# Performance work log

Hardware: AMD Instinct MI355X
Metric: run time of the kernel (lower is better)

Reference implementation:

```python
import jax, jax.numpy as jnp
import numpy as np

N, E, G = 100000, 400000, 4096
H, C = 4, 32            # heads, hidden_dim per head
D_OUT = H * C           # 128
NODE_D, EDGE_D = 38, 13
DEC_H, OUT_D = 64, 1
NEG_SLOPE = 0.2
LN_EPS = 1e-5


def setup_inputs() -> dict:
    key = jax.random.key(0)
    ks = jax.random.split(key, 40)
    r = lambda k, s: jax.random.normal(k, s, jnp.float32) * 0.1
    inp = {
        "x": jax.random.normal(ks[0], (N, NODE_D), jnp.float32),
        "edge_index": jax.random.randint(ks[1], (2, E), 0, N),
        "edge_attr": jax.random.uniform(ks[2], (E, EDGE_D), jnp.float32),
        "batch": jnp.sort(jax.random.randint(ks[3], (N,), 0, G)),
        # --- block 1 (in=38) ---
        "Wl1": r(ks[4], (NODE_D, D_OUT)), "bl1": jnp.zeros((D_OUT,), jnp.float32),
        "Wr1": r(ks[5], (NODE_D, D_OUT)), "br1": jnp.zeros((D_OUT,), jnp.float32),
        "We1": r(ks[6], (EDGE_D, D_OUT)),
        "att1": r(ks[7], (H, C)), "ab1": jnp.zeros((D_OUT,), jnp.float32),
        "ln_g1": jnp.ones((D_OUT,), jnp.float32), "ln_b1": jnp.zeros((D_OUT,), jnp.float32),
        "Wres": r(ks[8], (NODE_D, D_OUT)), "bres": jnp.zeros((D_OUT,), jnp.float32),
        # --- block 2 (in=128, residual = identity) ---
        "Wl2": r(ks[9], (D_OUT, D_OUT)), "bl2": jnp.zeros((D_OUT,), jnp.float32),
        "Wr2": r(ks[10], (D_OUT, D_OUT)), "br2": jnp.zeros((D_OUT,), jnp.float32),
        "We2": r(ks[11], (EDGE_D, D_OUT)),
        "att2": r(ks[12], (H, C)), "ab2": jnp.zeros((D_OUT,), jnp.float32),
        "ln_g2": jnp.ones((D_OUT,), jnp.float32), "ln_b2": jnp.zeros((D_OUT,), jnp.float32),
        # --- readout MLP ---
        "Wd1": r(ks[13], (D_OUT, DEC_H)), "bd1": jnp.zeros((DEC_H,), jnp.float32),
        "Wd2": r(ks[14], (DEC_H, OUT_D)), "bd2": jnp.zeros((OUT_D,), jnp.float32),
    }
    return inp


def _segment_softmax(logits, seg, n):
    m = jax.ops.segment_max(logits, seg, num_segments=n)
    ex = jnp.exp(logits - m[seg])
    s = jax.ops.segment_sum(ex, seg, num_segments=n)
    return ex / s[seg]


def _gatv2(x, src, dst, e_feat, Wl, bl, Wr, br, We, att, ab):
    n = x.shape[0]
    xl = (x @ Wl + bl).reshape(n, H, C)   # source transform
    xr = (x @ Wr + br).reshape(n, H, C)   # target transform
    ee = (e_feat @ We).reshape(-1, H, C)  # edge transform
    z = jax.nn.leaky_relu(xl[src] + xr[dst] + ee, NEG_SLOPE)  # [E,H,C]
    logits = jnp.einsum('ehc,hc->eh', z, att)                 # [E,H]
    alpha = _segment_softmax(logits, dst, n)                  # softmax over target nbhd
    out = jax.ops.segment_sum(xl[src] * alpha[..., None], dst, num_segments=n)
    return out.reshape(n, D_OUT) + ab


def _layernorm(h, g, b):
    mu = jnp.mean(h, -1, keepdims=True)
    d = h - mu
    v = jnp.mean(d * d, -1, keepdims=True)
    return d * jax.lax.rsqrt(v + LN_EPS) * g + b


def reference(x, edge_index, edge_attr, batch,
              Wl1, bl1, Wr1, br1, We1, att1, ab1, ln_g1, ln_b1, Wres, bres,
              Wl2, bl2, Wr2, br2, We2, att2, ab2, ln_g2, ln_b2,
              Wd1, bd1, Wd2, bd2):
    src, dst = edge_index[0], edge_index[1]
    n = x.shape[0]
    # add_self_loops(fill_value='mean'): self-loop edge attr = mean of incoming edge attrs
    deg = jax.ops.segment_sum(jnp.ones((src.shape[0],), x.dtype), dst, num_segments=n)
    loop_attr = jax.ops.segment_sum(edge_attr, dst, num_segments=n) / jnp.clip(deg, 1.0)[:, None]
    nodes = jnp.arange(n)
    src_a = jnp.concatenate([src, nodes])
    dst_a = jnp.concatenate([dst, nodes])
    ea = jnp.concatenate([edge_attr, loop_attr], axis=0)

    # block 1
    h = _gatv2(x, src_a, dst_a, ea, Wl1, bl1, Wr1, br1, We1, att1, ab1)
    h = jax.nn.elu(h)
    h = _layernorm(h + (x @ Wres + bres), ln_g1, ln_b1)
    # block 2 (identity residual)
    h2 = _gatv2(h, src_a, dst_a, ea, Wl2, bl2, Wr2, br2, We2, att2, ab2)
    h2 = jax.nn.elu(h2)
    h2 = _layernorm(h2 + h, ln_g2, ln_b2)

    # global mean pool over graphs
    cnt = jax.ops.segment_sum(jnp.ones((n,), x.dtype), batch, num_segments=G)
    g = jax.ops.segment_sum(h2, batch, num_segments=G) / jnp.clip(cnt, 1.0)[:, None]

    return jax.nn.relu(g @ Wd1 + bd1) @ Wd2 + bd2
```

## Files before the change

kernel.cpp:

```cpp
#include <hip/hip_runtime.h>

typedef unsigned short u16;
typedef unsigned int   u32;
typedef __attribute__((ext_vector_type(8))) short short8;
typedef __attribute__((ext_vector_type(4))) float float4v;
typedef __attribute__((ext_vector_type(2))) float float2v;
typedef __attribute__((ext_vector_type(4), aligned(4))) float float4u;

#define NODE_D   38
#define EDGE_D   13
#define D_OUT    128
#define NEG_SLOPE 0.2f
#define LN_EPS   1e-5f

__device__ __forceinline__ float bf2f(u16 v) { return __uint_as_float(((u32)v) << 16); }
__device__ __forceinline__ u16 f2bf(float f) {
    u32 u = __float_as_uint(f);
    u += 0x7fffu + ((u >> 16) & 1u);
    return (u16)(u >> 16);
}

template <int CTRL>
__device__ __forceinline__ float dpp_radd(float x) {
    int t = __builtin_amdgcn_update_dpp(0, __float_as_int(x), CTRL, 0xf, 0xf, true);
    return x + __int_as_float(t);
}
__device__ __forceinline__ float reduce16(float p) {
    p = dpp_radd<0xB1>(p);
    p = dpp_radd<0x4E>(p);
    p = dpp_radd<0x124>(p);
    p = dpp_radd<0x128>(p);
    return p;
}
__device__ __forceinline__ float reduce64(float v) {
    v = reduce16(v);
    v += __shfl_xor(v, 16, 64);
    v += __shfl_xor(v, 32, 64);
    return v;
}

__global__ void k_pre(const int* __restrict__ dst, int E, int* __restrict__ deg,
                      const int* __restrict__ batch, int N, int G, int* __restrict__ goff,
                      const float* __restrict__ x, u16* __restrict__ xb) {
    int i = blockIdx.x * blockDim.x + threadIdx.x;
    if (i < E) atomicAdd(deg + dst[i], 1);
    if (i < N) {
        int b = batch[i];
        int prev = (i == 0) ? -1 : batch[i - 1];
        for (int g = prev + 1; g <= b; g++) goff[g] = i;
        if (i == N - 1)
            for (int g = b + 1; g <= G; g++) goff[g] = N;
    }
    if (i < N * 32) {
        int n = i >> 5, kk = (i & 31) * 2;
        float f0 = 0.f, f1 = 0.f;
        if (kk < NODE_D) {
            float2v v = *(const float2v*)(x + (size_t)n * NODE_D + kk);
            f0 = v[0]; f1 = v[1];
        }
        ((u32*)xb)[(size_t)n * 32 + (i & 31)] = (u32)f2bf(f0) | ((u32)f2bf(f1) << 16);
    }
}

#define SCAN_CHUNK 1024
__global__ void k_scan1(const int* __restrict__ cnt, int N, int addone, int* __restrict__ bsum) {
    __shared__ int sh[256];
    int base = blockIdx.x * SCAN_CHUNK;
    int t = threadIdx.x;
    int s = 0;
#pragma unroll
    for (int i = 0; i < 4; i++) { int idx = base + t * 4 + i; if (idx < N) s += cnt[idx] + addone; }
    sh[t] = s; __syncthreads();
    for (int ofs = 128; ofs > 0; ofs >>= 1) {
        if (t < ofs) sh[t] += sh[t + ofs];
        __syncthreads();
    }
    if (t == 0) bsum[blockIdx.x] = sh[0];
}
__global__ void k_scan2(const int* __restrict__ bsum, int nb, int* __restrict__ boff) {
    __shared__ int sh[256];
    int t = threadIdx.x;
    if (nb <= 256) {
        int v = (t < nb) ? bsum[t] : 0;
        sh[t] = v; __syncthreads();
        for (int ofs = 1; ofs < 256; ofs <<= 1) {
            int x = (t >= ofs) ? sh[t - ofs] : 0;
            __syncthreads();
            sh[t] += x;
            __syncthreads();
        }
        if (t < nb) boff[t] = sh[t] - v;
        if (t == nb - 1) boff[nb] = sh[t];
    } else if (t == 0) {
        int run = 0;
        for (int i = 0; i < nb; i++) { boff[i] = run; run += bsum[i]; }
        boff[nb] = run;
    }
}
__global__ void k_scan3(const int* __restrict__ cnt, int N, int addone,
                        const int* __restrict__ boff, int nb, int* __restrict__ off) {
    __shared__ int wtot[4];
    int base = blockIdx.x * SCAN_CHUNK;
    int t = threadIdx.x;
    int lane = t & 63, w = t >> 6;
    int v[4]; int s = 0;
#pragma unroll
    for (int i = 0; i < 4; i++) { int idx = base + t * 4 + i; v[i] = (idx < N) ? cnt[idx] + addone : 0; s += v[i]; }
    int inc = s;
#pragma unroll
    for (int ofs = 1; ofs < 64; ofs <<= 1) {
        int x = __shfl_up(inc, ofs, 64);
        if (lane >= ofs) inc += x;
    }
    if (lane == 63) wtot[w] = inc;
    __syncthreads();
    int wofs = 0;
    for (int i = 0; i < w; i++) wofs += wtot[i];
    int run = boff[blockIdx.x] + wofs + (inc - s);
#pragma unroll
    for (int i = 0; i < 4; i++) {
        int idx = base + t * 4 + i;
        if (idx < N) off[idx] = run;
        run += v[i];
    }
    if (blockIdx.x == 0 && t == 0) off[N] = boff[nb];
}

__global__ void k_fill(const int* __restrict__ src, const int* __restrict__ dst,
                       const float* __restrict__ eattr, int E,
                       const int* __restrict__ csr_off, int* __restrict__ fill,
                       int* __restrict__ csr_src, u16* __restrict__ A) {
    int e = blockIdx.x * blockDim.x + threadIdx.x;
    if (e >= E) return;
    int d = dst[e];
    int pos = csr_off[d] + atomicAdd(fill + d, 1);
    csr_src[pos] = src[e];
    const float* ep = eattr + (size_t)e * EDGE_D;
    float4u v0 = *(const float4u*)(ep);
    float4u v1 = *(const float4u*)(ep + 4);
    float4u v2 = *(const float4u*)(ep + 8);
    float   v3 = ep[12];
    u16 row[16];
#pragma unroll
    for (int k = 0; k < 4; k++) { row[k] = f2bf(v0[k]); row[4 + k] = f2bf(v1[k]); row[8 + k] = f2bf(v2[k]); }
    row[12] = f2bf(v3);
#pragma unroll
    for (int k = EDGE_D; k < 16; k++) row[k] = 0;
    uint4* rp = (uint4*)(A + (size_t)pos * 16);
    rp[0] = (uint4){(u32)row[0] | ((u32)row[1] << 16), (u32)row[2] | ((u32)row[3] << 16),
                    (u32)row[4] | ((u32)row[5] << 16), (u32)row[6] | ((u32)row[7] << 16)};
    rp[1] = (uint4){(u32)row[8] | ((u32)row[9] << 16), (u32)row[10] | ((u32)row[11] << 16),
                    (u32)row[12] | ((u32)row[13] << 16), (u32)row[14] | ((u32)row[15] << 16)};
}

__global__ __launch_bounds__(256) void k_self(const int* __restrict__ csr_off, int N,
                                              int* __restrict__ csr_src, u16* __restrict__ A) {
    int wave = blockIdx.x * 4 + (threadIdx.x >> 6);
    if (wave >= N) return;
    int lane = threadIdx.x & 63;
    int r = lane >> 4, k = lane & 15;
    int b = csr_off[wave], e2 = csr_off[wave + 1] - 1;
    float s = 0.f;
    for (int j = b + r; j < e2; j += 4)
        s += bf2f(A[(size_t)j * 16 + k]);
    s += __shfl_xor(s, 16, 64);
    s += __shfl_xor(s, 32, 64);
    if (lane < 16) {
        u16 v = (k < EDGE_D) ? f2bf(s / fmaxf((float)(e2 - b), 1.f)) : (u16)0;
        A[(size_t)e2 * 16 + k] = v;
        if (k == 0) csr_src[e2] = wave;
    }
}

template <int KPAD, int CT, int KREAL, bool IN_BF16>
__global__ __launch_bounds__(256) void k_tf_mfma(
    const void* __restrict__ in_v,
    const float* __restrict__ W0, const float* __restrict__ b0,
    const float* __restrict__ W1, const float* __restrict__ b1,
    const float* __restrict__ W2, const float* __restrict__ b2,
    u16* __restrict__ o0, u16* __restrict__ o1, u16* __restrict__ o2,
    int N) {
    constexpr int RS = KPAD + 8;
    __shared__ u16 Bsw[CT * 16 * RS];
    __shared__ float bsh[CT * 16];
    const float* Ws[3] = {W0, W1, W2};
    const float* bs[3] = {b0, b1, b2};
    u16* outs[3] = {o0, o1, o2};
    int t = threadIdx.x;
    for (int i = t; i < CT * 16 * KPAD; i += 256) {
        int c = i / KPAD, k = i - c * KPAD;
        float v = (k < KREAL) ? Ws[c >> 7][(size_t)k * 128 + (c & 127)] : 0.f;
        Bsw[c * RS + k] = f2bf(v);
    }
    for (int i = t; i < CT * 16; i += 256) bsh[i] = bs[i >> 7][i & 127];
    __syncthreads();

    int wid = t >> 6, lane = t & 63;
    int quad = lane >> 4, m = lane & 15;

    for (int g0 = blockIdx.x * 64; g0 < N; g0 += gridDim.x * 64) {
        int na = g0 + wid * 16 + m;
        if (na > N - 1) na = N - 1;
        short8 a[KPAD / 32];
        if (IN_BF16) {
            const u16* in = (const u16*)in_v;
#pragma unroll
            for (int kc = 0; kc < KPAD / 32; kc++)
                a[kc] = *(const short8*)(in + (size_t)na * KPAD + kc * 32 + quad * 8);
        } else {
            const float* in = (const float*)in_v;
#pragma unroll
            for (int kc = 0; kc < KPAD / 32; kc++)
#pragma unroll
                for (int j = 0; j < 8; j++) {
                    int k = kc * 32 + quad * 8 + j;
                    float v = (k < KREAL) ? in[(size_t)na * KREAL + k] : 0.f;
                    a[kc][j] = (short)f2bf(v);
                }
        }
        float4v acc[CT];
#pragma unroll
        for (int ct = 0; ct < CT; ct++) acc[ct] = (float4v){0.f, 0.f, 0.f, 0.f};
#pragma unroll
        for (int ct = 0; ct < CT; ct++) {
#pragma unroll
            for (int kc = 0; kc < KPAD / 32; kc++) {
                short8 b = *(const short8*)(&Bsw[(ct * 16 + m) * RS + kc * 32 + quad * 8]);
                acc[ct] = __builtin_amdgcn_mfma_f32_16x16x32_bf16(b, a[kc], acc[ct], 0, 0, 0);
            }
        }
        int node = g0 + wid * 16 + m;
        if (node < N) {
#pragma unroll
            for (int ct = 0; ct < CT; ct++) {
                int colb = ct * 16 + quad * 4;
                u16* op = outs[colb >> 7];
                int cc = colb & 127;
                float4v bq = *(const float4v*)&bsh[colb];
                ushort4 wv;
                wv.x = f2bf(acc[ct][0] + bq[0]);
                wv.y = f2bf(acc[ct][1] + bq[1]);
                wv.z = f2bf(acc[ct][2] + bq[2]);
                wv.w = f2bf(acc[ct][3] + bq[3]);
                *(ushort4*)(op + (size_t)node * 128 + cc) = wv;
            }
        }
    }
}

template <bool POOL>
__global__ __launch_bounds__(256) void k_gat(
    const int* __restrict__ csr_off, const int* __restrict__ csr_src,
    const u16* __restrict__ A_csr,
    const u16* __restrict__ xl, const u16* __restrict__ xr,
    const u16* __restrict__ res, const float* __restrict__ We,
    const float* __restrict__ att, const float* __restrict__ ab,
    const float* __restrict__ lng, const float* __restrict__ lnb,
    u16* __restrict__ hout, const int* __restrict__ batch, float* __restrict__ gsum,
    int N, int npw) {
    int t = threadIdx.x;
    int wid = t >> 6, lane = t & 63;
    int nb = gridDim.x, b = blockIdx.x;
    int q = nb >> 3, r = nb & 7;
    int xcd = b & 7, ib = b >> 3;
    int swz = (xcd < r ? xcd * (q + 1) : r * (q + 1) + (xcd - r) * q) + ib;
    int wave = swz * 4 + wid;
    int n0 = wave * npw;
    if (n0 >= N) return;
    int n1 = n0 + npw; if (n1 > N) n1 = N;

    float2v we2[EDGE_D];
#pragma unroll
    for (int k = 0; k < EDGE_D; k++)
        we2[k] = (float2v){We[k * D_OUT + 2 * lane], We[k * D_OUT + 2 * lane + 1]};
    float a0 = att[2 * lane], a1 = att[2 * lane + 1];
    float abv0 = ab[2 * lane], abv1 = ab[2 * lane + 1];
    float lg0 = lng[2 * lane], lg1 = lng[2 * lane + 1];
    float lb0 = lnb[2 * lane], lb1 = lnb[2 * lane + 1];

    const u32* xl32 = (const u32*)xl;
    const u32* xr32 = (const u32*)xr;
    int wbeg = csr_off[n0];
    int wend = csr_off[n1];
    int nedge = wend - wbeg;

    float ps0 = 0.f, ps1 = 0.f;
    int gcur = POOL ? batch[n0] : -1;

    auto finish = [&](int n, float ssum, float2v acc2) {
        float inv = 1.f / ssum;
        float o0 = acc2[0] * inv + abv0;
        float o1 = acc2[1] * inv + abv1;
        o0 = (o0 > 0.f) ? o0 : (__expf(o0) - 1.f);
        o1 = (o1 > 0.f) ? o1 : (__expf(o1) - 1.f);
        u32 rw = ((const u32*)res)[(size_t)n * 64 + lane];
        o0 += bf2f((u16)(rw & 0xffff));
        o1 += bf2f((u16)(rw >> 16));
        float sm = reduce64(o0 + o1);
        float mu = sm * (1.f / 128.f);
        float d0 = o0 - mu, d1 = o1 - mu;
        float vv = reduce64(d0 * d0 + d1 * d1);
        float rs = rsqrtf(vv * (1.f / 128.f) + LN_EPS);
        float h0 = d0 * rs * lg0 + lb0;
        float h1 = d1 * rs * lg1 + lb1;
        if (POOL) {
            int g = batch[n];
            if (g != gcur) {
                atomicAdd(gsum + (size_t)gcur * 128 + 2 * lane, ps0);
                atomicAdd(gsum + (size_t)gcur * 128 + 2 * lane + 1, ps1);
                ps0 = 0.f; ps1 = 0.f; gcur = g;
            }
            ps0 += h0; ps1 += h1;
        } else {
            ((u32*)hout)[(size_t)n * 64 + lane] = (u32)f2bf(h0) | ((u32)f2bf(h1) << 16);
        }
    };

    const float2v z0v = (float2v){0.f, 0.f};

    if (nedge <= 64) {
        int last = nedge - 1;
        int sv = csr_src[wbeg + ((lane < nedge) ? lane : last)];
        int f0 = __builtin_amdgcn_readlane(sv, 0);
        int f1 = __builtin_amdgcn_readlane(sv, (1 <= last) ? 1 : last);
        int f2 = __builtin_amdgcn_readlane(sv, (2 <= last) ? 2 : last);
        int f3 = __builtin_amdgcn_readlane(sv, (3 <= last) ? 3 : last);
        u32 xw0 = xl32[(size_t)f0 * 64 + lane];
        u32 xw1 = xl32[(size_t)f1 * 64 + lane];
        u32 xw2 = xl32[(size_t)f2 * 64 + lane];
        u32 xw3 = xl32[(size_t)f3 * 64 + lane];
        int wbu = __builtin_amdgcn_readfirstlane(wbeg);
        const uint4* ap = (const uint4*)(A_csr + (size_t)wbu * 16);
        uint4 aq0 = ap[0], aq1 = ap[1];

        int i = wbeg;
        for (int n = n0; n < n1; n++) {
            int end = csr_off[n + 1];
            u32 xrw = xr32[(size_t)n * 64 + lane];
            float2v xr2 = (float2v){bf2f((u16)(xrw & 0xffff)), bf2f((u16)(xrw >> 16))};
            float ssum = 0.f;
            float2v acc2 = (float2v){0.f, 0.f};
            for (; i < end; i++) {
                int j4 = i + 4 - wbeg; if (j4 > last) j4 = last;
                int f4 = __builtin_amdgcn_readlane(sv, j4);
                u32 xwN = xl32[(size_t)f4 * 64 + lane];
                int j1n = i + 1 - wbeg; if (j1n > last) j1n = last;
                int ipu = __builtin_amdgcn_readfirstlane(wbeg + j1n);
                const uint4* apn = (const uint4*)(A_csr + (size_t)ipu * 16);
                uint4 an0 = apn[0], an1 = apn[1];

                u32 dw[8] = {aq0.x, aq0.y, aq0.z, aq0.w, aq1.x, aq1.y, aq1.z, aq1.w};
                float2v eeA = (float2v){0.f, 0.f}, eeB = (float2v){0.f, 0.f};
#pragma unroll
                for (int k = 0; k < EDGE_D; k++) {
                    u32 d = dw[k >> 1];
                    float av = __uint_as_float((k & 1) ? (d & 0xffff0000u) : (d << 16));
                    if ((k >> 1) & 1) eeB += we2[k] * av;
                    else             eeA += we2[k] * av;
                }
                float2v xs = (float2v){bf2f((u16)(xw0 & 0xffff)), bf2f((u16)(xw0 >> 16))};
                float2v z = (xs + xr2) + (eeA + eeB);
                float2v lz = __builtin_elementwise_max(z, z0v) + __builtin_elementwise_min(z, z0v) * NEG_SLOPE;
                float p = lz[0] * a0 + lz[1] * a1;
                p = reduce16(p);
                float wgt = __expf(p);
                ssum += wgt;
                acc2 += xs * wgt;
                xw0 = xw1; xw1 = xw2; xw2 = xw3; xw3 = xwN;
                aq0 = an0; aq1 = an1;
            }
            finish(n, ssum, acc2);
        }
    } else {
        int cl = wend - 1;
        int f = csr_src[wbeg];
        u32 xw = xl32[(size_t)f * 64 + lane];
        int wbu = __builtin_amdgcn_readfirstlane(wbeg);
        const uint4* ap = (const uint4*)(A_csr + (size_t)wbu * 16);
        uint4 aq0 = ap[0], aq1 = ap[1];
        int i = wbeg;
        for (int n = n0; n < n1; n++) {
            int end = csr_off[n + 1];
            u32 xrw = xr32[(size_t)n * 64 + lane];
            float2v xr2 = (float2v){bf2f((u16)(xrw & 0xffff)), bf2f((u16)(xrw >> 16))};
            float ssum = 0.f;
            float2v acc2 = (float2v){0.f, 0.f};
            for (; i < end; i++) {
                u32 xwc = xw; uint4 q0 = aq0, q1 = aq1;
                int ip = (i + 1 < wend) ? i + 1 : cl;
                f = csr_src[ip];
                xw = xl32[(size_t)f * 64 + lane];
                int ipu = __builtin_amdgcn_readfirstlane(ip);
                const uint4* ap2 = (const uint4*)(A_csr + (size_t)ipu * 16);
                aq0 = ap2[0]; aq1 = ap2[1];
                u32 dw[8] = {q0.x, q0.y, q0.z, q0.w, q1.x, q1.y, q1.z, q1.w};
                float2v eeA = (float2v){0.f, 0.f}, eeB = (float2v){0.f, 0.f};
#pragma unroll
                for (int k = 0; k < EDGE_D; k++) {
                    u32 d = dw[k >> 1];
                    float av = __uint_as_float((k & 1) ? (d & 0xffff0000u) : (d << 16));
                    if ((k >> 1) & 1) eeB += we2[k] * av;
                    else             eeA += we2[k] * av;
                }
                float2v xs = (float2v){bf2f((u16)(xwc & 0xffff)), bf2f((u16)(xwc >> 16))};
                float2v z = (xs + xr2) + (eeA + eeB);
                float2v lz = __builtin_elementwise_max(z, z0v) + __builtin_elementwise_min(z, z0v) * NEG_SLOPE;
                float p = lz[0] * a0 + lz[1] * a1;
                p = reduce16(p);
                float wgt = __expf(p);
                ssum += wgt;
                acc2 += xs * wgt;
            }
            finish(n, ssum, acc2);
        }
    }

    if (POOL) {
        atomicAdd(gsum + (size_t)gcur * 128 + 2 * lane, ps0);
        atomicAdd(gsum + (size_t)gcur * 128 + 2 * lane + 1, ps1);
    }
}

__global__ __launch_bounds__(128) void k_read(
    const float* __restrict__ gsum, const int* __restrict__ goff,
    const float* __restrict__ Wd1, const float* __restrict__ bd1,
    const float* __restrict__ Wd2, const float* __restrict__ bd2,
    float* __restrict__ out, int G) {
    __shared__ float psh[128];
    __shared__ float rsh[2][64];
    int g = blockIdx.x;
    int t = threadIdx.x;
    int cnt = goff[g + 1] - goff[g];
    float inv = 1.f / fmaxf((float)cnt, 1.f);
    psh[t] = gsum[(size_t)g * 128 + t] * inv;
    __syncthreads();
    int j = t & 63, hw = t >> 6;
    float acc = (hw == 0) ? bd1[j] : 0.f;
    int k0 = hw * 64;
    for (int k = k0; k < k0 + 64; k++)
        acc += psh[k] * Wd1[k * 64 + j];
    rsh[hw][j] = acc;
    __syncthreads();
    if (t < 64) {
        float a = fmaxf(rsh[0][t] + rsh[1][t], 0.f);
        float v = a * Wd2[t];
#pragma unroll
        for (int mk = 1; mk < 64; mk <<= 1) v += __shfl_xor(v, mk, 64);
        if (t == 0) out[g] = v + bd2[0];
    }
}

extern "C" void kernel_launch(void* const* d_in, const int* in_sizes, int n_in,
                              void* d_out, int out_size, void* d_ws, size_t ws_size,
                              hipStream_t stream) {
    const float* x     = (const float*)d_in[0];
    const int*   eidx  = (const int*)d_in[1];
    const float* eattr = (const float*)d_in[2];
    const int*   batch = (const int*)d_in[3];
    const float* Wl1 = (const float*)d_in[4],  *bl1 = (const float*)d_in[5];
    const float* Wr1 = (const float*)d_in[6],  *br1 = (const float*)d_in[7];
    const float* We1 = (const float*)d_in[8],  *att1 = (const float*)d_in[9],  *ab1 = (const float*)d_in[10];
    const float* lng1 = (const float*)d_in[11], *lnb1 = (const float*)d_in[12];
    const float* Wres = (const float*)d_in[13], *bres = (const float*)d_in[14];
    const float* Wl2 = (const float*)d_in[15], *bl2 = (const float*)d_in[16];
    const float* Wr2 = (const float*)d_in[17], *br2 = (const float*)d_in[18];
    const float* We2 = (const float*)d_in[19], *att2 = (const float*)d_in[20], *ab2 = (const float*)d_in[21];
    const float* lng2 = (const float*)d_in[22], *lnb2 = (const float*)d_in[23];
    const float* Wd1 = (const float*)d_in[24], *bd1 = (const float*)d_in[25];
    const float* Wd2 = (const float*)d_in[26], *bd2 = (const float*)d_in[27];

    int N = in_sizes[0] / NODE_D;
    int E = in_sizes[1] / 2;
    int G = out_size;
    int EN = E + N;
    const int* src = eidx;
    const int* dst = eidx + E;

    char* w = (char*)d_ws;
    auto alloc = [&](size_t bytes) -> char* {
        char* p = w;
        w += (bytes + 255) & ~(size_t)255;
        return p;
    };
    int NB = (N + SCAN_CHUNK - 1) / SCAN_CHUNK;
    int*   csr_off  = (int*)alloc((size_t)(N + 1) * 4);
    int*   csr_src  = (int*)alloc((size_t)EN * 4);
    u16*   A_csr    = (u16*)alloc((size_t)(EN + 64) * 16 * 2);
    u16*   xb       = (u16*)alloc((size_t)N * 64 * 2);
    u16*   xlb      = (u16*)alloc((size_t)N * D_OUT * 2);
    u16*   xrb      = (u16*)alloc((size_t)N * D_OUT * 2);
    u16*   resb     = (u16*)alloc((size_t)N * D_OUT * 2);
    u16*   hb       = (u16*)alloc((size_t)N * D_OUT * 2);
    int*   goff     = (int*)alloc((size_t)(G + 1) * 4);
    size_t szN = ((size_t)N * 4 + 255) & ~(size_t)255;
    size_t szG = ((size_t)G * 128 * 4 + 255) & ~(size_t)255;
    char*  zp   = alloc(2 * szN + szG);
    int*   deg  = (int*)zp;
    int*   fill = (int*)(zp + szN);
    float* gsum = (float*)(zp + 2 * szN);
    int*   bsum = (int*)alloc((size_t)(NB + 1) * 4);
    int*   boff = (int*)alloc((size_t)(NB + 1) * 4);

    hipMemsetAsync(zp, 0, 2 * szN + szG, stream);

    int mx = (E > N * 32) ? E : N * 32;
    k_pre<<<(mx + 255) / 256, 256, 0, stream>>>(dst, E, deg, batch, N, G, goff, x, xb);

    k_scan1<<<NB, 256, 0, stream>>>(deg, N, 1, bsum);
    k_scan2<<<1, 256, 0, stream>>>(bsum, NB, boff);
    k_scan3<<<NB, 256, 0, stream>>>(deg, N, 1, boff, NB, csr_off);
    k_fill<<<(E + 255) / 256, 256, 0, stream>>>(src, dst, eattr, E, csr_off, fill, csr_src, A_csr);
    k_self<<<(N + 3) / 4, 256, 0, stream>>>(csr_off, N, csr_src, A_csr);

    int npw = 4;
    int gblocks = (N + npw * 4 - 1) / (npw * 4);

    k_tf_mfma<64, 24, NODE_D, true><<<512, 256, 0, stream>>>(
        xb, Wl1, bl1, Wr1, br1, Wres, bres, xlb, xrb, resb, N);
    k_gat<false><<<gblocks, 256, 0, stream>>>(csr_off, csr_src, A_csr,
                                              xlb, xrb, resb, We1, att1, ab1, lng1, lnb1,
                                              hb, nullptr, nullptr, N, npw);

    k_tf_mfma<128, 16, 128, true><<<512, 256, 0, stream>>>(
        hb, Wl2, bl2, Wr2, br2, Wr2, br2, xlb, xrb, xrb, N);
    k_gat<true><<<gblocks, 256, 0, stream>>>(csr_off, csr_src, A_csr,
                                             xlb, xrb, hb, We2, att2, ab2, lng2, lnb2,
                                             (u16*)nullptr, batch, gsum, N, npw);

    k_read<<<G, 128, 0, stream>>>(gsum, goff, Wd1, bd1, Wd2, bd2, (float*)d_out, G);
}
```

Measured before the change: 549.1 us.

## Split GATv2 attention logit computation into separate edge-parallel kernel

Adds a k_logit kernel that computes per-edge, per-head exp(attention logit) in edge-parallel fashion and writes them to a weight buffer. The aggregation kernel k_gat then only reads those weights and gathers xl, with a deeper 8-deep source prefetch, and the XCD block swizzle is dropped. The aim is to take the dependent edge-feature math off the per-node serial loop and balance work across edges. The cost is an extra launch per layer, a stored dst_csr array, and write plus reread traffic for the weight buffer, and xl is gathered twice per edge.

```diff
diff --git a/kernel.cpp b/kernel.cpp
--- a/kernel.cpp
+++ b/kernel.cpp
@@ -12,6 +12,7 @@
 #define D_OUT    128
 #define NEG_SLOPE 0.2f
 #define LN_EPS   1e-5f
+#define SPW      4
 
 __device__ __forceinline__ float bf2f(u16 v) { return __uint_as_float(((u32)v) << 16); }
 __device__ __forceinline__ u16 f2bf(float f) {
@@ -129,12 +130,14 @@
 __global__ void k_fill(const int* __restrict__ src, const int* __restrict__ dst,
                        const float* __restrict__ eattr, int E,
                        const int* __restrict__ csr_off, int* __restrict__ fill,
-                       int* __restrict__ csr_src, u16* __restrict__ A) {
+                       int* __restrict__ csr_src, int* __restrict__ dst_csr,
+                       u16* __restrict__ A) {
     int e = blockIdx.x * blockDim.x + threadIdx.x;
     if (e >= E) return;
     int d = dst[e];
     int pos = csr_off[d] + atomicAdd(fill + d, 1);
     csr_src[pos] = src[e];
+    dst_csr[pos] = d;
     const float* ep = eattr + (size_t)e * EDGE_D;
     float4u v0 = *(const float4u*)(ep);
     float4u v1 = *(const float4u*)(ep + 4);
@@ -154,7 +157,8 @@
 }
 
 __global__ __launch_bounds__(256) void k_self(const int* __restrict__ csr_off, int N,
-                                              int* __restrict__ csr_src, u16* __restrict__ A) {
+                                              int* __restrict__ csr_src, int* __restrict__ dst_csr,
+                                              u16* __restrict__ A) {
     int wave = blockIdx.x * 4 + (threadIdx.x >> 6);
     if (wave >= N) return;
     int lane = threadIdx.x & 63;
@@ -168,7 +172,7 @@
     if (lane < 16) {
         u16 v = (k < EDGE_D) ? f2bf(s / fmaxf((float)(e2 - b), 1.f)) : (u16)0;
         A[(size_t)e2 * 16 + k] = v;
-        if (k == 0) csr_src[e2] = wave;
+        if (k == 0) { csr_src[e2] = wave; dst_csr[e2] = wave; }
     }
 }
 
@@ -248,38 +252,76 @@
     }
 }
 
+__global__ __launch_bounds__(256) void k_logit(
+    const int* __restrict__ csr_src, const int* __restrict__ dst_csr,
+    const u16* __restrict__ A_csr,
+    const u16* __restrict__ xl, const u16* __restrict__ xr,
+    const float* __restrict__ We, const float* __restrict__ att,
+    float* __restrict__ wvec, int nslots) {
+    int lane = threadIdx.x & 63;
+    int w = __builtin_amdgcn_readfirstlane(blockIdx.x * 4 + (threadIdx.x >> 6));
+    int j0 = w * SPW;
+    if (j0 >= nslots) return;
+    int jend = j0 + SPW; if (jend > nslots) jend = nslots;
+
+    float2v we2[EDGE_D];
+#pragma unroll
+    for (int k = 0; k < EDGE_D; k++)
+        we2[k] = (float2v){We[k * D_OUT + 2 * lane], We[k * D_OUT + 2 * lane + 1]};
+    float a0 = att[2 * lane], a1 = att[2 * lane + 1];
+    const u32* xl32 = (const u32*)xl;
+    const u32* xr32 = (const u32*)xr;
+    const float2v z0v = (float2v){0.f, 0.f};
+
+    for (int j = j0; j < jend; j++) {
+        int src = csr_src[j];
+        int dn  = dst_csr[j];
+        u32 xw  = xl32[(size_t)src * 64 + lane];
+        u32 xrw = xr32[(size_t)dn * 64 + lane];
+        const uint4* ap = (const uint4*)(A_csr + (size_t)j * 16);
+        uint4 q0 = ap[0], q1 = ap[1];
+        u32 dw[8] = {q0.x, q0.y, q0.z, q0.w, q1.x, q1.y, q1.z, q1.w};
+        float2v eeA = (float2v){0.f, 0.f}, eeB = (float2v){0.f, 0.f};
+#pragma unroll
+        for (int k = 0; k < EDGE_D; k++) {
+            u32 d = dw[k >> 1];
+            float av = __uint_as_float((k & 1) ? (d & 0xffff0000u) : (d << 16));
+            if ((k >> 1) & 1) eeB += we2[k] * av;
+            else             eeA += we2[k] * av;
+        }
+        float2v xs  = (float2v){bf2f((u16)(xw & 0xffff)), bf2f((u16)(xw >> 16))};
+        float2v xr2 = (float2v){bf2f((u16)(xrw & 0xffff)), bf2f((u16)(xrw >> 16))};
+        float2v z = (xs + xr2) + (eeA + eeB);
+        float2v lz = __builtin_elementwise_max(z, z0v) + __builtin_elementwise_min(z, z0v) * NEG_SLOPE;
+        float p = lz[0] * a0 + lz[1] * a1;
+        p = reduce16(p);
+        float wgt = __expf(p);
+        if ((lane & 15) == 0) wvec[(size_t)j * 4 + (lane >> 4)] = wgt;
+    }
+}
+
 template <bool POOL>
 __global__ __launch_bounds__(256) void k_gat(
     const int* __restrict__ csr_off, const int* __restrict__ csr_src,
-    const u16* __restrict__ A_csr,
-    const u16* __restrict__ xl, const u16* __restrict__ xr,
-    const u16* __restrict__ res, const float* __restrict__ We,
-    const float* __restrict__ att, const float* __restrict__ ab,
+    const float* __restrict__ wvec,
+    const u16* __restrict__ xl, const u16* __restrict__ res,
+    const float* __restrict__ ab,
     const float* __restrict__ lng, const float* __restrict__ lnb,
     u16* __restrict__ hout, const int* __restrict__ batch, float* __restrict__ gsum,
     int N, int npw) {
     int t = threadIdx.x;
     int wid = t >> 6, lane = t & 63;
-    int nb = gridDim.x, b = blockIdx.x;
-    int q = nb >> 3, r = nb & 7;
-    int xcd = b & 7, ib = b >> 3;
-    int swz = (xcd < r ? xcd * (q + 1) : r * (q + 1) + (xcd - r) * q) + ib;
-    int wave = swz * 4 + wid;
+    int wave = blockIdx.x * 4 + wid;
     int n0 = wave * npw;
     if (n0 >= N) return;
     int n1 = n0 + npw; if (n1 > N) n1 = N;
 
-    float2v we2[EDGE_D];
-#pragma unroll
-    for (int k = 0; k < EDGE_D; k++)
-        we2[k] = (float2v){We[k * D_OUT + 2 * lane], We[k * D_OUT + 2 * lane + 1]};
-    float a0 = att[2 * lane], a1 = att[2 * lane + 1];
     float abv0 = ab[2 * lane], abv1 = ab[2 * lane + 1];
     float lg0 = lng[2 * lane], lg1 = lng[2 * lane + 1];
     float lb0 = lnb[2 * lane], lb1 = lnb[2 * lane + 1];
+    int hd = lane >> 4;
 
     const u32* xl32 = (const u32*)xl;
-    const u32* xr32 = (const u32*)xr;
     int wbeg = csr_off[n0];
     int wend = csr_off[n1];
     int nedge = wend - wbeg;
@@ -316,58 +358,44 @@
         }
     };
 
-    const float2v z0v = (float2v){0.f, 0.f};
-
     if (nedge <= 64) {
         int last = nedge - 1;
         int sv = csr_src[wbeg + ((lane < nedge) ? lane : last)];
-        int f0 = __builtin_amdgcn_readlane(sv, 0);
-        int f1 = __builtin_amdgcn_readlane(sv, (1 <= last) ? 1 : last);
-        int f2 = __builtin_amdgcn_readlane(sv, (2 <= last) ? 2 : last);
-        int f3 = __builtin_amdgcn_readlane(sv, (3 <= last) ? 3 : last);
-        u32 xw0 = xl32[(size_t)f0 * 64 + lane];
-        u32 xw1 = xl32[(size_t)f1 * 64 + lane];
-        u32 xw2 = xl32[(size_t)f2 * 64 + lane];
-        u32 xw3 = xl32[(size_t)f3 * 64 + lane];
-        int wbu = __builtin_amdgcn_readfirstlane(wbeg);
-        const uint4* ap = (const uint4*)(A_csr + (size_t)wbu * 16);
-        uint4 aq0 = ap[0], aq1 = ap[1];
+        u32 xw[8];
+        float wg[4];
+#pragma unroll
+        for (int r = 0; r < 8; r++) {
+            int jr = (r <= last) ? r : last;
+            int fr = __builtin_amdgcn_readlane(sv, jr);
+            xw[r] = xl32[(size_t)fr * 64 + lane];
+        }
+#pragma unroll
+        for (int r = 0; r < 4; r++) {
+            int jr = (r <= last) ? r : last;
+            wg[r] = wvec[(size_t)(wbeg + jr) * 4 + hd];
+        }
 
         int i = wbeg;
         for (int n = n0; n < n1; n++) {
             int end = csr_off[n + 1];
-            u32 xrw = xr32[(size_t)n * 64 + lane];
-            float2v xr2 = (float2v){bf2f((u16)(xrw & 0xffff)), bf2f((u16)(xrw >> 16))};
             float ssum = 0.f;
             float2v acc2 = (float2v){0.f, 0.f};
             for (; i < end; i++) {
+                int j8 = i + 8 - wbeg; if (j8 > last) j8 = last;
+                int f8 = __builtin_amdgcn_readlane(sv, j8);
+                u32 xwN = xl32[(size_t)f8 * 64 + lane];
                 int j4 = i + 4 - wbeg; if (j4 > last) j4 = last;
-                int f4 = __builtin_amdgcn_readlane(sv, j4);
-                u32 xwN = xl32[(size_t)f4 * 64 + lane];
-                int j1n = i + 1 - wbeg; if (j1n > last) j1n = last;
-                int ipu = __builtin_amdgcn_readfirstlane(wbeg + j1n);
-                const uint4* apn = (const uint4*)(A_csr + (size_t)ipu * 16);
-                uint4 an0 = apn[0], an1 = apn[1];
-
-                u32 dw[8] = {aq0.x, aq0.y, aq0.z, aq0.w, aq1.x, aq1.y, aq1.z, aq1.w};
-                float2v eeA = (float2v){0.f, 0.f}, eeB = (float2v){0.f, 0.f};
-#pragma unroll
-                for (int k = 0; k < EDGE_D; k++) {
-                    u32 d = dw[k >> 1];
-                    float av = __uint_as_float((k & 1) ? (d & 0xffff0000u) : (d << 16));
-                    if ((k >> 1) & 1) eeB += we2[k] * av;
-                    else             eeA += we2[k] * av;
-                }
-                float2v xs = (float2v){bf2f((u16)(xw0 & 0xffff)), bf2f((u16)(xw0 >> 16))};
-                float2v z = (xs + xr2) + (eeA + eeB);
-                float2v lz = __builtin_elementwise_max(z, z0v) + __builtin_elementwise_min(z, z0v) * NEG_SLOPE;
-                float p = lz[0] * a0 + lz[1] * a1;
-                p = reduce16(p);
-                float wgt = __expf(p);
-                ssum += wgt;
-                acc2 += xs * wgt;
-                xw0 = xw1; xw1 = xw2; xw2 = xw3; xw3 = xwN;
-                aq0 = an0; aq1 = an1;
+                float wgN = wvec[(size_t)(wbeg + j4) * 4 + hd];
+
+                float2v xs = (float2v){bf2f((u16)(xw[0] & 0xffff)), bf2f((u16)(xw[0] >> 16))};
+                ssum += wg[0];
+                acc2 += xs * wg[0];
+#pragma unroll
+                for (int r = 0; r < 7; r++) xw[r] = xw[r + 1];
+                xw[7] = xwN;
+#pragma unroll
+                for (int r = 0; r < 3; r++) wg[r] = wg[r + 1];
+                wg[3] = wgN;
             }
             finish(n, ssum, acc2);
         }
@@ -375,41 +403,21 @@
         int cl = wend - 1;
         int f = csr_src[wbeg];
         u32 xw = xl32[(size_t)f * 64 + lane];
-        int wbu = __builtin_amdgcn_readfirstlane(wbeg);
-        const uint4* ap = (const uint4*)(A_csr + (size_t)wbu * 16);
-        uint4 aq0 = ap[0], aq1 = ap[1];
+        float wg = wvec[(size_t)wbeg * 4 + hd];
         int i = wbeg;
         for (int n = n0; n < n1; n++) {
             int end = csr_off[n + 1];
-            u32 xrw = xr32[(size_t)n * 64 + lane];
-            float2v xr2 = (float2v){bf2f((u16)(xrw & 0xffff)), bf2f((u16)(xrw >> 16))};
             float ssum = 0.f;
             float2v acc2 = (float2v){0.f, 0.f};
             for (; i < end; i++) {
-                u32 xwc = xw; uint4 q0 = aq0, q1 = aq1;
+                u32 xwc = xw; float wgc = wg;
                 int ip = (i + 1 < wend) ? i + 1 : cl;
                 f = csr_src[ip];
                 xw = xl32[(size_t)f * 64 + lane];
-                int ipu = __builtin_amdgcn_readfirstlane(ip);
-                const uint4* ap2 = (const uint4*)(A_csr + (size_t)ipu * 16);
-                aq0 = ap2[0]; aq1 = ap2[1];
-                u32 dw[8] = {q0.x, q0.y, q0.z, q0.w, q1.x, q1.y, q1.z, q1.w};
-                float2v eeA = (float2v){0.f, 0.f}, eeB = (float2v){0.f, 0.f};
-#pragma unroll
-                for (int k = 0; k < EDGE_D; k++) {
-                    u32 d = dw[k >> 1];
-                    float av = __uint_as_float((k & 1) ? (d & 0xffff0000u) : (d << 16));
-                    if ((k >> 1) & 1) eeB += we2[k] * av;
-                    else             eeA += we2[k] * av;
-                }
+                wg = wvec[(size_t)ip * 4 + hd];
                 float2v xs = (float2v){bf2f((u16)(xwc & 0xffff)), bf2f((u16)(xwc >> 16))};
-                float2v z = (xs + xr2) + (eeA + eeB);
-                float2v lz = __builtin_elementwise_max(z, z0v) + __builtin_elementwise_min(z, z0v) * NEG_SLOPE;
-                float p = lz[0] * a0 + lz[1] * a1;
-                p = reduce16(p);
-                float wgt = __expf(p);
-                ssum += wgt;
-                acc2 += xs * wgt;
+                ssum += wgc;
+                acc2 += xs * wgc;
             }
             finish(n, ssum, acc2);
         }
@@ -485,7 +493,9 @@
     int NB = (N + SCAN_CHUNK - 1) / SCAN_CHUNK;
     int*   csr_off  = (int*)alloc((size_t)(N + 1) * 4);
     int*   csr_src  = (int*)alloc((size_t)EN * 4);
+    int*   dst_csr  = (int*)alloc((size_t)EN * 4);
     u16*   A_csr    = (u16*)alloc((size_t)(EN + 64) * 16 * 2);
+    float* wvec     = (float*)alloc((size_t)EN * 4 * 4);
     u16*   xb       = (u16*)alloc((size_t)N * 64 * 2);
     u16*   xlb      = (u16*)alloc((size_t)N * D_OUT * 2);
     u16*   xrb      = (u16*)alloc((size_t)N * D_OUT * 2);
@@ -509,22 +519,26 @@
     k_scan1<<<NB, 256, 0, stream>>>(deg, N, 1, bsum);
     k_scan2<<<1, 256, 0, stream>>>(bsum, NB, boff);
     k_scan3<<<NB, 256, 0, stream>>>(deg, N, 1, boff, NB, csr_off);
-    k_fill<<<(E + 255) / 256, 256, 0, stream>>>(src, dst, eattr, E, csr_off, fill, csr_src, A_csr);
-    k_self<<<(N + 3) / 4, 256, 0, stream>>>(csr_off, N, csr_src, A_csr);
+    k_fill<<<(E + 255) / 256, 256, 0, stream>>>(src, dst, eattr, E, csr_off, fill, csr_src, dst_csr, A_csr);
+    k_self<<<(N + 3) / 4, 256, 0, stream>>>(csr_off, N, csr_src, dst_csr, A_csr);
 
     int npw = 4;
     int gblocks = (N + npw * 4 - 1) / (npw * 4);
+    int lwaves = (EN + SPW - 1) / SPW;
+    int lblocks = (lwaves + 3) / 4;
 
     k_tf_mfma<64, 24, NODE_D, true><<<512, 256, 0, stream>>>(
         xb, Wl1, bl1, Wr1, br1, Wres, bres, xlb, xrb, resb, N);
-    k_gat<false><<<gblocks, 256, 0, stream>>>(csr_off, csr_src, A_csr,
-                                              xlb, xrb, resb, We1, att1, ab1, lng1, lnb1,
+    k_logit<<<lblocks, 256, 0, stream>>>(csr_src, dst_csr, A_csr, xlb, xrb, We1, att1, wvec, EN);
+    k_gat<false><<<gblocks, 256, 0, stream>>>(csr_off, csr_src, wvec,
+                                              xlb, resb, ab1, lng1, lnb1,
                                               hb, nullptr, nullptr, N, npw);
 
     k_tf_mfma<128, 16, 128, true><<<512, 256, 0, stream>>>(
         hb, Wl2, bl2, Wr2, br2, Wr2, br2, xlb, xrb, xrb, N);
-    k_gat<true><<<gblocks, 256, 0, stream>>>(csr_off, csr_src, A_csr,
-                                             xlb, xrb, hb, We2, att2, ab2, lng2, lnb2,
+    k_logit<<<lblocks, 256, 0, stream>>>(csr_src, dst_csr, A_csr, xlb, xrb, We2, att2, wvec, EN);
+    k_gat<true><<<gblocks, 256, 0, stream>>>(csr_off, csr_src, wvec,
+                                             xlb, hb, ab2, lng2, lnb2,
                                              (u16*)nullptr, batch, gsum, N, npw);
 
     k_read<<<G, 128, 0, stream>>>(gsum, goff, Wd1, bd1, Wd2, bd2, (float*)d_out, G);
```

Result: slower. 563.0 us (+2.5%).
